# Kernel optimization log

Hardware: AMD Instinct MI355X
Metric: run time of the kernel (lower is better)

Reference implementation:

```python
import jax, jax.numpy as jnp
import numpy as np

T, H, W, B = 9, 128, 128, 8  # size=[9,128,128], 8 samples in batch
N = 4194304


def _avg3(x):
    # AvgPool3d(kernel=(1,3,3), stride=1, pad=(0,1,1), count_include_pad=True)
    s = jax.lax.reduce_window(x, 0.0, jax.lax.add, (1, 1, 1, 3, 3), (1, 1, 1, 1, 1),
                              ((0, 0), (0, 0), (0, 0), (1, 1), (1, 1)))
    return s / 9.0


def _inorm(x, eps=1e-5):
    # InstanceNorm3d(affine=False): normalize over (T,H,W) per sample/channel
    m = x.mean(axis=(2, 3, 4), keepdims=True)
    v = x.var(axis=(2, 3, 4), keepdims=True)
    return (x - m) * jax.lax.rsqrt(v + eps)


def _time_corr(x):
    bx = (x > 0).astype(x.dtype)
    bx = jnp.concatenate([bx, bx[:, :, -1:]], axis=2)  # ReplicationPad3d back in T
    prev = _avg3(bx)
    around = (prev[:, :, :-1] * bx[:, :, 1:] > 4.0 / 9.0).astype(x.dtype)
    return _avg3(around)


def _dyn_conv(x, fc1_w, fc2_w, dyn_w):
    # Dynamic_Conv, kernel (3,1,1): attention over k=4 weight banks, per-sample conv
    a = x.mean(axis=(2, 3, 4))                       # [B,C] global avg pool
    a = jax.nn.relu(a @ fc1_w.T)
    a = jax.nn.softmax(a @ fc2_w.T, axis=1)          # [B,k]
    w = jnp.einsum('bk,koid->boid', a, dyn_w)        # [B,O,I,3]
    xp = jnp.pad(x, ((0, 0), (0, 0), (1, 1), (0, 0), (0, 0)))  # pad T
    t = x.shape[2]
    out = jnp.einsum('boi,bithw->bothw', w[..., 0], xp[:, :, 0:t])
    out = out + jnp.einsum('boi,bithw->bothw', w[..., 1], xp[:, :, 1:1 + t])
    out = out + jnp.einsum('boi,bithw->bothw', w[..., 2], xp[:, :, 2:2 + t])
    return out


def _voxelize(t, x, y, p, b):
    # per-batch normalize t by max, then bilinear-in-time scatter-add over T bins
    tmax = jax.ops.segment_max(t, b, num_segments=B)
    ts = (t / tmax[b]) * T                                         # [N]
    bins = jnp.arange(T, dtype=ts.dtype)
    vals = jnp.maximum(1.0 - jnp.abs(ts[None, :] - bins[:, None]), 0.0)  # [T,N]
    base = x + W * y + W * H * T * p + 2 * W * H * T * b           # [N]
    idx = base[None, :] + W * H * jnp.arange(T, dtype=base.dtype)[:, None]
    vox = jnp.zeros(B * 2 * T * H * W, dtype=ts.dtype).at[idx].add(vals)
    return vox.reshape(B, 2, T, H, W)


def setup_inputs() -> dict:
    key = jax.random.key(0)
    ks = jax.random.split(key, 10)
    t = jax.random.uniform(ks[0], (N,), dtype=jnp.float32)
    x = jax.random.randint(ks[1], (N,), 0, W, dtype=jnp.int32)
    y = jax.random.randint(ks[2], (N,), 0, H, dtype=jnp.int32)
    p = jax.random.randint(ks[3], (N,), 0, 2, dtype=jnp.int32)
    b = jnp.sort(jax.random.randint(ks[4], (N,), 0, B, dtype=jnp.int32))
    conv1_w = jax.random.normal(ks[5], (16, 2), jnp.float32) / np.sqrt(2.0)
    fc1_w = jax.random.normal(ks[6], (8, 16), jnp.float32) / np.sqrt(16.0)
    fc2_w = jax.random.normal(ks[7], (4, 8), jnp.float32) / np.sqrt(8.0)
    dyn_w = jax.random.normal(ks[8], (4, 16, 16, 3), jnp.float32) / np.sqrt(48.0)
    conv3_w = jax.random.normal(ks[9], (2, 16), jnp.float32) / np.sqrt(16.0)
    return {"t": t, "x": x, "y": y, "p": p, "b": b,
            "conv1_w": conv1_w, "fc1_w": fc1_w, "fc2_w": fc2_w,
            "dyn_w": dyn_w, "conv3_w": conv3_w}


def reference(t, x, y, p, b, conv1_w, fc1_w, fc2_w, dyn_w, conv3_w):
    vox = _voxelize(t, x, y, p, b)                     # [B,2,T,H,W]
    mask = _time_corr(vox)
    h = _inorm(vox)
    h = jnp.einsum('oc,bcthw->bothw', conv1_w, h)      # 1x1x1 conv 2->16
    h = _dyn_conv(h, fc1_w, fc2_w, dyn_w)
    h = jnp.einsum('oc,bcthw->bothw', conv3_w, h)      # 1x1x1 conv 16->2
    out = _inorm(jax.nn.sigmoid(h) * mask)
    return out
```

## Files before the change

kernel.cpp:

```cpp
#include <hip/hip_runtime.h>
#include <math.h>

#define TT 9
#define HH 128
#define WW 128
#define BB 8
#define SLICE (HH*WW)
#define CHW (TT*SLICE)
#define BCH (2*CHW)
#define TOT (BB*BCH)
#define INV_M (1.0f/147456.0f)
#define NYG 16
#define NBK (9*NYG)
#define SEGCAP 8192u
#define SSCALE 274877906944.0f
#define INV_SSCALE (1.0/274877906944.0)

__global__ void __launch_bounds__(1024) k_bounds(
        const int* __restrict__ b, int* __restrict__ start, int n,
        const float* __restrict__ conv1_w, const float* __restrict__ dyn_w,
        const float* __restrict__ conv3_w, float* __restrict__ Kc,
        unsigned* __restrict__ tailz, unsigned* __restrict__ cursor, int initCur) {
    if (blockIdx.x == 1) {
        if (threadIdx.x < 72) tailz[threadIdx.x] = 0u;
        if (initCur)
            for (int i = threadIdx.x; i < 8 * NBK; i += 1024)
                cursor[i] = (unsigned)i * SEGCAP;
        return;
    }
    int tid = threadIdx.x;
    if (tid < 9) {
        if (tid == 0) start[0] = 0;
        else if (tid == 8) start[8] = n;
        else {
            int lo = 0, hi = n;
            while (lo < hi) { int mid = (lo + hi) >> 1; if (b[mid] < tid) lo = mid + 1; else hi = mid; }
            start[tid] = lo;
        }
    }
    if (tid >= 32 && tid < 44) {
        int q = tid - 32;
        int d = q % 3, c = (q / 3) & 1, o2 = q / 6;
        float acc = 0.0f;
        for (int o = 0; o < 16; ++o) {
            float c3 = conv3_w[o2 * 16 + o];
            for (int i = 0; i < 16; ++i) {
                float wsum = 0.0f;
                for (int k = 0; k < 4; ++k) wsum += dyn_w[((k * 16 + o) * 16 + i) * 3 + d];
                acc += c3 * (0.25f * wsum) * conv1_w[i * 2 + c];
            }
        }
        Kc[q] = acc;
    }
}

__global__ void __launch_bounds__(1024) k_tmax(
        const float* __restrict__ t, const int* __restrict__ start,
        unsigned* __restrict__ gmax) {
    __shared__ unsigned sm[1024];
    int bi = blockIdx.x & 7, cj = blockIdx.x >> 3, nb = gridDim.x >> 3;
    int s = start[bi], e = start[bi + 1];
    unsigned m = 0u;
    if (e > s) {
        int a = (s + 3) & ~3; if (a > e) a = e;
        int z = e & ~3;       if (z < a) z = a;
        if (cj == 0) {
            int i = s + (int)threadIdx.x;
            if (i < a) { unsigned v = __float_as_uint(t[i]); if (v > m) m = v; }
            i = z + (int)threadIdx.x;
            if (i < e) { unsigned v = __float_as_uint(t[i]); if (v > m) m = v; }
        }
        long nq = (long)(z - a) >> 2;
        long per = (nq + nb - 1) / nb;
        long q0 = (long)cj * per; if (q0 > nq) q0 = nq;
        long q1 = q0 + per;       if (q1 > nq) q1 = nq;
        const float4* tp = (const float4*)(t + a);
        for (long i = q0 + threadIdx.x; i < q1; i += 1024) {
            float4 u = tp[i];
            unsigned c = __float_as_uint(fmaxf(fmaxf(u.x, u.y), fmaxf(u.z, u.w)));
            if (c > m) m = c;
        }
    }
    sm[threadIdx.x] = m;
    __syncthreads();
    for (int ofs = 512; ofs > 0; ofs >>= 1) {
        if (threadIdx.x < ofs && sm[threadIdx.x + ofs] > sm[threadIdx.x])
            sm[threadIdx.x] = sm[threadIdx.x + ofs];
        __syncthreads();
    }
    if (threadIdx.x == 0 && sm[0]) atomicMax(&gmax[bi], sm[0]);
}

__global__ void __launch_bounds__(1024) k_place(
        const float* __restrict__ t, const int* __restrict__ x,
        const int* __restrict__ y, const int* __restrict__ p,
        const unsigned* __restrict__ gmax, const int* __restrict__ start,
        unsigned* __restrict__ cursor, int2* __restrict__ rec) {
    __shared__ unsigned lh[NBK], lc[NBK], cbase[NBK];
    __shared__ unsigned wsum[3];
    __shared__ int2 srec[4096];
    __shared__ unsigned char sbkt[4096];
    int bi = blockIdx.x & 7, cj = blockIdx.x >> 3, nb = gridDim.x >> 3;
    int s = start[bi], e = start[bi + 1];
    if (e <= s) return;
    float tmax = __uint_as_float(gmax[bi]);
    int a = (s + 3) & ~3; if (a > e) a = e;
    int z = e & ~3;       if (z < a) z = a;
    long nq = (long)(z - a) >> 2;
    long per = (nq + nb - 1) / nb;
    long q0 = (long)cj * per; if (q0 > nq) q0 = nq;
    long q1 = q0 + per;       if (q1 > nq) q1 = nq;
    const float4* tp = (const float4*)(t + a);
    const int4*   xp = (const int4*)(x + a);
    const int4*   yp = (const int4*)(y + a);
    const int4*   pp = (const int4*)(p + a);
    for (long base = q0; base < q1; base += 1024) {
        if (threadIdx.x < NBK) lh[threadIdx.x] = 0u;
        __syncthreads();
        long qi = base + threadIdx.x;
        int lb[4]; float tsv[4]; int keyv[4]; unsigned rank[4];
        #pragma unroll
        for (int k = 0; k < 4; ++k) lb[k] = -1;
        if (qi < q1) {
            float4 tv = tp[qi]; int4 xv = xp[qi]; int4 yv = yp[qi]; int4 pv = pp[qi];
            float tq[4] = {tv.x, tv.y, tv.z, tv.w};
            int   xq[4] = {xv.x, xv.y, xv.z, xv.w};
            int   yq[4] = {yv.x, yv.y, yv.z, yv.w};
            int   pq[4] = {pv.x, pv.y, pv.z, pv.w};
            #pragma unroll
            for (int k = 0; k < 4; ++k) {
                float ts = tq[k] / tmax * 9.0f;
                int i0 = (int)floorf(ts);
                if ((unsigned)i0 < 9u) {
                    lb[k] = i0 * NYG + (yq[k] >> 3);
                    tsv[k] = ts;
                    keyv[k] = xq[k] + (yq[k] << 7) + (pq[k] << 14);
                }
            }
        }
        #pragma unroll
        for (int k = 0; k < 4; ++k)
            if (lb[k] >= 0) rank[k] = atomicAdd(&lh[lb[k]], 1u);
        __syncthreads();
        unsigned v = 0, inc = 0;
        if (threadIdx.x < 192) {
            v = (threadIdx.x < NBK) ? lh[threadIdx.x] : 0u;
            inc = v;
            #pragma unroll
            for (int ofs = 1; ofs < 64; ofs <<= 1) {
                unsigned u = __shfl_up(inc, ofs, 64);
                if ((threadIdx.x & 63) >= ofs) inc += u;
            }
            if ((threadIdx.x & 63) == 63) wsum[threadIdx.x >> 6] = inc;
        }
        __syncthreads();
        if (threadIdx.x < NBK) {
            unsigned ex = inc - v;
            int w = threadIdx.x >> 6;
            if (w >= 1) ex += wsum[0];
            if (w >= 2) ex += wsum[1];
            cbase[threadIdx.x] = ex;
            lc[threadIdx.x] = v ? atomicAdd(&cursor[bi * NBK + threadIdx.x], v) : 0u;
        }
        __syncthreads();
        #pragma unroll
        for (int k = 0; k < 4; ++k)
            if (lb[k] >= 0) {
                unsigned sl_ = cbase[lb[k]] + rank[k];
                srec[sl_] = make_int2(__float_as_int(tsv[k]), keyv[k]);
                sbkt[sl_] = (unsigned char)lb[k];
            }
        __syncthreads();
        unsigned tot = cbase[NBK - 1] + lh[NBK - 1];
        #pragma unroll
        for (int h = 0; h < 4; ++h) {
            unsigned slot = threadIdx.x + h * 1024;
            if (slot < tot) {
                int bkt = sbkt[slot];
                unsigned dst = lc[bkt] + (slot - cbase[bkt]);
                if (dst < (unsigned)(bi * NBK + bkt + 1) * SEGCAP)
                    rec[dst] = srec[slot];
            }
        }
        __syncthreads();
    }
    if (cj == 0) {
        int i = -1;
        if ((int)threadIdx.x < a - s) i = s + threadIdx.x;
        else if (threadIdx.x >= 64 && (int)(threadIdx.x - 64) < e - z) i = z + (threadIdx.x - 64);
        if (i >= 0) {
            float ts = t[i] / tmax * 9.0f;
            int i0 = (int)floorf(ts);
            if ((unsigned)i0 < 9u) {
                int lbx = i0 * NYG + (y[i] >> 3);
                unsigned slot = atomicAdd(&cursor[bi * NBK + lbx], 1u);
                if (slot < (unsigned)(bi * NBK + lbx + 1) * SEGCAP)
                    rec[slot] = make_int2(__float_as_int(ts), x[i] + (y[i] << 7) + (p[i] << 14));
            }
        }
    }
}

#define CELL(K) (((K) & 1023) | (((K) >> 4) & 1024))
#define DEP1(TSB, KEY) { float ts_ = __int_as_float(TSB); \
    unsigned long long sq_ = (unsigned long long)(ts_ * SSCALE); \
    atomicAdd(&asl[CELL(KEY)], (1ull << 48) | sq_); }

__global__ void __launch_bounds__(1024) k_accum(
        const int2* __restrict__ rec, const unsigned* __restrict__ cursor,
        unsigned long long* __restrict__ Abuf) {
    __shared__ unsigned long long asl[2048];
    int tg = blockIdx.x, bb = blockIdx.y, yg = blockIdx.z;
    asl[threadIdx.x] = 0ull; asl[1024 + threadIdx.x] = 0ull;
    __syncthreads();
    int lb = bb * NBK + tg * NYG + yg;
    unsigned s = (unsigned)lb * SEGCAP;
    unsigned e = cursor[lb];
    unsigned cap = s + SEGCAP; if (e > cap) e = cap;
    unsigned a = (s + 1) & ~1u, z = e & ~1u; if (z < a) z = a;
    if (threadIdx.x == 0 && s < a && s < e) { int2 r = rec[s]; DEP1(r.x, r.y) }
    if (threadIdx.x == 1 && z < e)          { int2 r = rec[z]; DEP1(r.x, r.y) }
    int n2 = (int)((z - a) >> 1);
    const int4* rp = (const int4*)(rec + a);
    for (int i = threadIdx.x; i < n2; i += 1024) {
        int4 q = rp[i];
        DEP1(q.x, q.y)
        DEP1(q.z, q.w)
    }
    __syncthreads();
    unsigned long long* Ao = Abuf + s;
    Ao[threadIdx.x]        = asl[threadIdx.x];
    Ao[1024 + threadIdx.x] = asl[1024 + threadIdx.x];
}

__global__ void __launch_bounds__(256) k_recon(
        const unsigned long long* __restrict__ Abuf,
        float* __restrict__ vox, float* __restrict__ s1) {
    int idx = blockIdx.x * 256 + threadIdx.x;
    int cell = idx & 2047;
    int yg = (idx >> 11) & 15;
    int bb = idx >> 15;
    unsigned long long Av[9];
    #pragma unroll
    for (int t = 0; t < 9; ++t)
        Av[t] = Abuf[(size_t)(unsigned)(bb * NBK + t * NYG + yg) * SEGCAP + cell];
    int p = cell >> 10, row = (cell >> 7) & 7, xx = cell & 127;
    float* vp = vox + (size_t)bb * BCH + (size_t)p * CHW + (size_t)(((yg << 3) + row) << 7) + xx;
    double Cp = 0.0, Sp = 0.0;
    float ls = 0.f, lq = 0.f;
    #pragma unroll
    for (int t = 0; t < 9; ++t) {
        double C = (double)(unsigned)(Av[t] >> 48);
        double S = (double)(Av[t] & 0xFFFFFFFFFFFFull) * INV_SSCALE;
        float v = (float)(C * (double)(1 + t) - S + (Sp - Cp * (double)(t - 1)));
        vp[t * SLICE] = v;
        ls += v; lq += v * v;
        Cp = C; Sp = S;
    }
    __shared__ float ss[256], sq[256];
    ss[threadIdx.x] = ls; sq[threadIdx.x] = lq;
    __syncthreads();
    for (int ofs = 128; ofs > 0; ofs >>= 1) {
        if (threadIdx.x < ofs) { ss[threadIdx.x] += ss[threadIdx.x + ofs]; sq[threadIdx.x] += sq[threadIdx.x + ofs]; }
        __syncthreads();
    }
    if (threadIdx.x == 0) {
        int bc = bb * 2 + p;
        atomicAdd(&s1[bc], ss[0]); atomicAdd(&s1[16 + bc], sq[0]);
    }
}

__global__ void __launch_bounds__(1024, 4) k_scat(
        const float* __restrict__ t, const int* __restrict__ x,
        const int* __restrict__ y, const int* __restrict__ p,
        const unsigned* __restrict__ gmax, const int* __restrict__ start,
        float* __restrict__ vox) {
    __shared__ float sl[2 * SLICE];
    int tg = blockIdx.x, bb = blockIdx.y;
    int cs = start[bb], ce = start[bb + 1];
    for (int j = threadIdx.x; j < 2 * SLICE; j += 1024) sl[j] = 0.0f;
    __syncthreads();
    float tmax = __uint_as_float(gmax[bb]);
    float ftg = (float)tg;
    for (int i = cs + threadIdx.x; i < ce; i += 1024) {
        float ts = t[i] / tmax * 9.0f;
        float fl = floorf(ts);
        int i0 = (int)fl;
        bool h0 = (i0 == tg), h1 = (i0 + 1 == tg);
        if (h0 | h1) {
            float w = h0 ? (1.0f - (ts - fl)) : (1.0f - (ftg - ts));
            int hw = x[i] + (y[i] << 7) + (p[i] << 14);
            atomicAdd(&sl[hw], w);
        }
    }
    __syncthreads();
    float* dst = vox + (size_t)bb * BCH + (size_t)tg * SLICE;
    for (int j = threadIdx.x; j < SLICE; j += 1024) {
        dst[j]       = sl[j];
        dst[CHW + j] = sl[SLICE + j];
    }
}

__global__ void k_stats1(const float* __restrict__ vox, float* __restrict__ s1) {
    __shared__ float ss[256], sq[256];
    int bc = blockIdx.x >> 5, part = blockIdx.x & 31;
    const float4* vp = (const float4*)(vox + (long)bc * CHW);
    const int per = (CHW / 4) / 32;
    float s = 0.f, q = 0.f;
    for (int j = part * per + threadIdx.x; j < (part + 1) * per; j += 256) {
        float4 v = vp[j];
        s += v.x + v.y + v.z + v.w;
        q += v.x * v.x + v.y * v.y + v.z * v.z + v.w * v.w;
    }
    ss[threadIdx.x] = s; sq[threadIdx.x] = q;
    __syncthreads();
    for (int ofs = 128; ofs > 0; ofs >>= 1) {
        if (threadIdx.x < ofs) { ss[threadIdx.x] += ss[threadIdx.x + ofs]; sq[threadIdx.x] += sq[threadIdx.x + ofs]; }
        __syncthreads();
    }
    if (threadIdx.x == 0) { atomicAdd(&s1[bc], ss[0]); atomicAdd(&s1[16 + bc], sq[0]); }
}

#define STRIP 32
__global__ void k_mask(const float* __restrict__ vox, float* __restrict__ mask) {
    __shared__ unsigned char sbx[36 * 128];
    __shared__ unsigned char sar[34 * 128];
    int bid = blockIdx.x;
    int strip = bid & 3;
    int t = (bid >> 2) % 9;
    int c = (bid / 36) & 1;
    int bb = bid / 72;
    long off = (long)bb * BCH + (long)c * CHW;
    const float* vt = vox + off + (long)t * SLICE;
    int tn = (t + 1 < 9) ? t + 1 : 8;
    const float* vn = vox + off + (long)tn * SLICE;
    int y0 = strip * STRIP;
    for (int j = threadIdx.x; j < 36 * 128; j += 256) {
        int r = j >> 7, xx = j & 127;
        int gy = y0 - 2 + r;
        sbx[j] = ((unsigned)gy < 128u && vt[(gy << 7) + xx] > 0.0f) ? 1 : 0;
    }
    __syncthreads();
    for (int j = threadIdx.x; j < 34 * 128; j += 256) {
        int ra = j >> 7, xx = j & 127;
        int gy = y0 - 1 + ra;
        unsigned char v = 0;
        if ((unsigned)gy < 128u) {
            int s = 0;
            for (int rs = ra; rs <= ra + 2; ++rs)
                for (int dx = -1; dx <= 1; ++dx) {
                    int x2 = xx + dx; if ((unsigned)x2 >= 128u) continue;
                    s += sbx[(rs << 7) + x2];
                }
            v = (vn[(gy << 7) + xx] > 0.0f && s >= 5) ? 1 : 0;
        }
        sar[j] = v;
    }
    __syncthreads();
    float* mt = mask + off + (long)t * SLICE;
    for (int j = threadIdx.x; j < STRIP * 128; j += 256) {
        int q = j >> 7, xx = j & 127;
        int s = 0;
        for (int ra = q; ra <= q + 2; ++ra)
            for (int dx = -1; dx <= 1; ++dx) {
                int x2 = xx + dx; if ((unsigned)x2 >= 128u) continue;
                s += sar[(ra << 7) + x2];
            }
        mt[((y0 + q) << 7) + xx] = (float)s / 9.0f;
    }
}

__global__ void __launch_bounds__(256) k_g(
        const float* __restrict__ vox, float* __restrict__ gm,
        const float* __restrict__ s1, const float* __restrict__ Kc,
        float* __restrict__ s2) {
    __shared__ float snrm[32];
    if (threadIdx.x < 16) {
        float mm = s1[threadIdx.x] * INV_M;
        float var = s1[16 + threadIdx.x] * INV_M - mm * mm;
        float inv = rsqrtf(var + 1e-5f);
        snrm[threadIdx.x] = inv;
        snrm[16 + threadIdx.x] = -mm * inv;
    }
    __syncthreads();
    int idx = blockIdx.x * 256 + threadIdx.x;
    int hw = idx & (SLICE - 1);
    int o2 = (idx >> 14) & 1;
    int bb = idx >> 15;
    const float* v0 = vox + (size_t)bb * BCH + hw;
    const float* v1 = v0 + CHW;
    float* go = gm + (size_t)bb * BCH + (size_t)o2 * CHW + hw;
    float a[9], d[9], m[9];
    #pragma unroll
    for (int tt = 0; tt < 9; ++tt) a[tt] = v0[tt * SLICE];
    #pragma unroll
    for (int tt = 0; tt < 9; ++tt) d[tt] = v1[tt * SLICE];
    #pragma unroll
    for (int tt = 0; tt < 9; ++tt) m[tt] = go[tt * SLICE];
    float sc0 = snrm[bb * 2], sh0 = snrm[16 + bb * 2];
    float sc1 = snrm[bb * 2 + 1], sh1 = snrm[16 + bb * 2 + 1];
    float k00 = Kc[o2 * 6 + 0], k01 = Kc[o2 * 6 + 1], k02 = Kc[o2 * 6 + 2];
    float k10 = Kc[o2 * 6 + 3], k11 = Kc[o2 * 6 + 4], k12 = Kc[o2 * 6 + 5];
    #pragma unroll
    for (int tt = 0; tt < 9; ++tt) { a[tt] = a[tt] * sc0 + sh0; d[tt] = d[tt] * sc1 + sh1; }
    float ls = 0.f, lq = 0.f;
    #pragma unroll
    for (int tt = 0; tt < 9; ++tt) {
        float pre = k01 * a[tt] + k11 * d[tt];
        if (tt > 0) pre += k00 * a[tt - 1] + k10 * d[tt - 1];
        if (tt < 8) pre += k02 * a[tt + 1] + k12 * d[tt + 1];
        float sig = 1.0f / (1.0f + expf(-pre));
        float g = sig * m[tt];
        go[tt * SLICE] = g;
        ls += g; lq += g * g;
    }
    __shared__ float ss[256], sq[256];
    ss[threadIdx.x] = ls; sq[threadIdx.x] = lq;
    __syncthreads();
    for (int ofs = 128; ofs > 0; ofs >>= 1) {
        if (threadIdx.x < ofs) { ss[threadIdx.x] += ss[threadIdx.x + ofs]; sq[threadIdx.x] += sq[threadIdx.x + ofs]; }
        __syncthreads();
    }
    if (threadIdx.x == 0) {
        int bc = bb * 2 + o2;
        atomicAdd(&s2[bc], ss[0]); atomicAdd(&s2[16 + bc], sq[0]);
    }
}

__global__ void k_norm(float* __restrict__ out, const float* __restrict__ s2) {
    int i4 = blockIdx.x * 256 + threadIdx.x;
    int bc = i4 / (CHW / 4);
    float m = s2[bc] * INV_M;
    float var = s2[16 + bc] * INV_M - m * m;
    float inv = rsqrtf(var + 1e-5f);
    float4 v = ((float4*)out)[i4];
    v.x = (v.x - m) * inv; v.y = (v.y - m) * inv;
    v.z = (v.z - m) * inv; v.w = (v.w - m) * inv;
    ((float4*)out)[i4] = v;
}

extern "C" void kernel_launch(void* const* d_in, const int* in_sizes, int n_in,
                              void* d_out, int out_size, void* d_ws, size_t ws_size,
                              hipStream_t stream) {
    const float* t  = (const float*)d_in[0];
    const int*   x  = (const int*)d_in[1];
    const int*   y  = (const int*)d_in[2];
    const int*   p  = (const int*)d_in[3];
    const int*   b  = (const int*)d_in[4];
    const float* conv1_w = (const float*)d_in[5];
    const float* dyn_w   = (const float*)d_in[8];
    const float* conv3_w = (const float*)d_in[9];
    float* out = (float*)d_out;
    int n = in_sizes[0];

    const long RECF = 2L * 8 * NBK * SEGCAP;
    long availF = (long)(ws_size / sizeof(float));
    long need = (long)TOT + RECF + 4096;
    int useBuckets = (availF >= need);

    float* ws   = (float*)d_ws;
    float* vox  = ws;
    int2*  rec  = (int2*)(ws + TOT);
    float* tail = ws + TOT + (useBuckets ? RECF : 0);
    unsigned* gmax    = (unsigned*)tail;
    float*    s1      = tail + 8;
    float*    s2      = tail + 40;
    float*    Kc      = tail + 72;
    int*      start   = (int*)(tail + 84);
    unsigned* cursor  = (unsigned*)(tail + 96);

    k_bounds<<<2, 1024, 0, stream>>>(b, start, n, conv1_w, dyn_w, conv3_w, Kc,
                                     (unsigned*)tail, cursor, useBuckets);
    k_tmax<<<256, 1024, 0, stream>>>(t, start, gmax);
    if (useBuckets) {
        k_place<<<512, 1024, 0, stream>>>(t, x, y, p, gmax, start, cursor, rec);
        k_accum<<<dim3(9, 8, NYG), 1024, 0, stream>>>(rec, cursor,
                                                      (unsigned long long*)rec);
        k_recon<<<1024, 256, 0, stream>>>((const unsigned long long*)rec, vox, s1);
    } else {
        k_scat<<<dim3(9, 8, 1), 1024, 0, stream>>>(t, x, y, p, gmax, start, vox);
        k_stats1<<<512, 256, 0, stream>>>(vox, s1);
    }
    k_mask<<<576, 256, 0, stream>>>(vox, out);
    k_g<<<1024, 256, 0, stream>>>(vox, out, s1, Kc, s2);
    k_norm<<<TOT / 1024, 256, 0, stream>>>(out, s2);
}
```

Measured before the change: 134.8 us.

## Fuse bucket accumulation and voxel reconstruction into one kernel looping over time

Merges k_accum and k_recon into k_accum9. Each block now owns one batch and one 4-row y-group and walks all nine time bins in turn, accumulating into LDS and writing voxel values and partial statistics straight from shared memory. This removes the 64-bit accumulator round trip through global memory and one kernel launch. To fit the LDS tile, bucketing changes to 32 y-groups with half the segment capacity, which means 2-byte bucket ids and a wider prefix scan in k_place. The trade-off is a smaller grid (256 blocks instead of 1152) with serial per-bin loops and extra barriers.

```diff
diff --git a/kernel.cpp b/kernel.cpp
--- a/kernel.cpp
+++ b/kernel.cpp
@@ -10,9 +10,9 @@
 #define BCH (2*CHW)
 #define TOT (BB*BCH)
 #define INV_M (1.0f/147456.0f)
-#define NYG 16
+#define NYG 32
 #define NBK (9*NYG)
-#define SEGCAP 8192u
+#define SEGCAP 4096u
 #define SSCALE 274877906944.0f
 #define INV_SSCALE (1.0/274877906944.0)
 
@@ -97,9 +97,9 @@
         const unsigned* __restrict__ gmax, const int* __restrict__ start,
         unsigned* __restrict__ cursor, int2* __restrict__ rec) {
     __shared__ unsigned lh[NBK], lc[NBK], cbase[NBK];
-    __shared__ unsigned wsum[3];
+    __shared__ unsigned wsum[5];
     __shared__ int2 srec[4096];
-    __shared__ unsigned char sbkt[4096];
+    __shared__ unsigned short sbkt[4096];
     int bi = blockIdx.x & 7, cj = blockIdx.x >> 3, nb = gridDim.x >> 3;
     int s = start[bi], e = start[bi + 1];
     if (e <= s) return;
@@ -132,7 +132,7 @@
                 float ts = tq[k] / tmax * 9.0f;
                 int i0 = (int)floorf(ts);
                 if ((unsigned)i0 < 9u) {
-                    lb[k] = i0 * NYG + (yq[k] >> 3);
+                    lb[k] = i0 * NYG + (yq[k] >> 2);
                     tsv[k] = ts;
                     keyv[k] = xq[k] + (yq[k] << 7) + (pq[k] << 14);
                 }
@@ -143,7 +143,7 @@
             if (lb[k] >= 0) rank[k] = atomicAdd(&lh[lb[k]], 1u);
         __syncthreads();
         unsigned v = 0, inc = 0;
-        if (threadIdx.x < 192) {
+        if (threadIdx.x < 320) {
             v = (threadIdx.x < NBK) ? lh[threadIdx.x] : 0u;
             inc = v;
             #pragma unroll
@@ -157,8 +157,7 @@
         if (threadIdx.x < NBK) {
             unsigned ex = inc - v;
             int w = threadIdx.x >> 6;
-            if (w >= 1) ex += wsum[0];
-            if (w >= 2) ex += wsum[1];
+            for (int j = 0; j < w; ++j) ex += wsum[j];
             cbase[threadIdx.x] = ex;
             lc[threadIdx.x] = v ? atomicAdd(&cursor[bi * NBK + threadIdx.x], v) : 0u;
         }
@@ -168,7 +167,7 @@
             if (lb[k] >= 0) {
                 unsigned sl_ = cbase[lb[k]] + rank[k];
                 srec[sl_] = make_int2(__float_as_int(tsv[k]), keyv[k]);
-                sbkt[sl_] = (unsigned char)lb[k];
+                sbkt[sl_] = (unsigned short)lb[k];
             }
         __syncthreads();
         unsigned tot = cbase[NBK - 1] + lh[NBK - 1];
@@ -192,7 +191,7 @@
             float ts = t[i] / tmax * 9.0f;
             int i0 = (int)floorf(ts);
             if ((unsigned)i0 < 9u) {
-                int lbx = i0 * NYG + (y[i] >> 3);
+                int lbx = i0 * NYG + (y[i] >> 2);
                 unsigned slot = atomicAdd(&cursor[bi * NBK + lbx], 1u);
                 if (slot < (unsigned)(bi * NBK + lbx + 1) * SEGCAP)
                     rec[slot] = make_int2(__float_as_int(ts), x[i] + (y[i] << 7) + (p[i] << 14));
@@ -201,73 +200,61 @@
     }
 }
 
-#define CELL(K) (((K) & 1023) | (((K) >> 4) & 1024))
+#define CELL(K) (((K) & 511) | (((K) >> 5) & 512))
 #define DEP1(TSB, KEY) { float ts_ = __int_as_float(TSB); \
     unsigned long long sq_ = (unsigned long long)(ts_ * SSCALE); \
     atomicAdd(&asl[CELL(KEY)], (1ull << 48) | sq_); }
 
-__global__ void __launch_bounds__(1024) k_accum(
+__global__ void __launch_bounds__(1024) k_accum9(
         const int2* __restrict__ rec, const unsigned* __restrict__ cursor,
-        unsigned long long* __restrict__ Abuf) {
-    __shared__ unsigned long long asl[2048];
-    int tg = blockIdx.x, bb = blockIdx.y, yg = blockIdx.z;
-    asl[threadIdx.x] = 0ull; asl[1024 + threadIdx.x] = 0ull;
-    __syncthreads();
-    int lb = bb * NBK + tg * NYG + yg;
-    unsigned s = (unsigned)lb * SEGCAP;
-    unsigned e = cursor[lb];
-    unsigned cap = s + SEGCAP; if (e > cap) e = cap;
-    unsigned a = (s + 1) & ~1u, z = e & ~1u; if (z < a) z = a;
-    if (threadIdx.x == 0 && s < a && s < e) { int2 r = rec[s]; DEP1(r.x, r.y) }
-    if (threadIdx.x == 1 && z < e)          { int2 r = rec[z]; DEP1(r.x, r.y) }
-    int n2 = (int)((z - a) >> 1);
-    const int4* rp = (const int4*)(rec + a);
-    for (int i = threadIdx.x; i < n2; i += 1024) {
-        int4 q = rp[i];
-        DEP1(q.x, q.y)
-        DEP1(q.z, q.w)
-    }
-    __syncthreads();
-    unsigned long long* Ao = Abuf + s;
-    Ao[threadIdx.x]        = asl[threadIdx.x];
-    Ao[1024 + threadIdx.x] = asl[1024 + threadIdx.x];
-}
-
-__global__ void __launch_bounds__(256) k_recon(
-        const unsigned long long* __restrict__ Abuf,
         float* __restrict__ vox, float* __restrict__ s1) {
-    int idx = blockIdx.x * 256 + threadIdx.x;
-    int cell = idx & 2047;
-    int yg = (idx >> 11) & 15;
-    int bb = idx >> 15;
-    unsigned long long Av[9];
-    #pragma unroll
-    for (int t = 0; t < 9; ++t)
-        Av[t] = Abuf[(size_t)(unsigned)(bb * NBK + t * NYG + yg) * SEGCAP + cell];
-    int p = cell >> 10, row = (cell >> 7) & 7, xx = cell & 127;
-    float* vp = vox + (size_t)bb * BCH + (size_t)p * CHW + (size_t)(((yg << 3) + row) << 7) + xx;
+    __shared__ unsigned long long asl[1024];
+    __shared__ float rs[1024], rq[1024];
+    int bb = blockIdx.x, yg = blockIdx.y;
+    int cell = threadIdx.x;
+    int pch = cell >> 9, row = (cell >> 7) & 3, xx = cell & 127;
+    float* vp = vox + (size_t)bb * BCH + (size_t)pch * CHW
+              + (size_t)(((yg << 2) + row) << 7) + xx;
     double Cp = 0.0, Sp = 0.0;
     float ls = 0.f, lq = 0.f;
-    #pragma unroll
     for (int t = 0; t < 9; ++t) {
-        double C = (double)(unsigned)(Av[t] >> 48);
-        double S = (double)(Av[t] & 0xFFFFFFFFFFFFull) * INV_SSCALE;
+        asl[cell] = 0ull;
+        __syncthreads();
+        int lb = bb * NBK + t * NYG + yg;
+        unsigned s = (unsigned)lb * SEGCAP;
+        unsigned e = cursor[lb];
+        unsigned cap = s + SEGCAP; if (e > cap) e = cap;
+        unsigned a = (s + 1) & ~1u, z = e & ~1u; if (z < a) z = a;
+        if (threadIdx.x == 0 && s < a && s < e) { int2 r = rec[s]; DEP1(r.x, r.y) }
+        if (threadIdx.x == 1 && z < e)          { int2 r = rec[z]; DEP1(r.x, r.y) }
+        int n2 = (int)((z - a) >> 1);
+        const int4* rp = (const int4*)(rec + a);
+        for (int i = threadIdx.x; i < n2; i += 1024) {
+            int4 q = rp[i];
+            DEP1(q.x, q.y)
+            DEP1(q.z, q.w)
+        }
+        __syncthreads();
+        unsigned long long Av = asl[cell];
+        double C = (double)(unsigned)(Av >> 48);
+        double S = (double)(Av & 0xFFFFFFFFFFFFull) * INV_SSCALE;
         float v = (float)(C * (double)(1 + t) - S + (Sp - Cp * (double)(t - 1)));
         vp[t * SLICE] = v;
         ls += v; lq += v * v;
         Cp = C; Sp = S;
-    }
-    __shared__ float ss[256], sq[256];
-    ss[threadIdx.x] = ls; sq[threadIdx.x] = lq;
-    __syncthreads();
-    for (int ofs = 128; ofs > 0; ofs >>= 1) {
-        if (threadIdx.x < ofs) { ss[threadIdx.x] += ss[threadIdx.x + ofs]; sq[threadIdx.x] += sq[threadIdx.x + ofs]; }
-        __syncthreads();
-    }
-    if (threadIdx.x == 0) {
-        int bc = bb * 2 + p;
-        atomicAdd(&s1[bc], ss[0]); atomicAdd(&s1[16 + bc], sq[0]);
-    }
+        __syncthreads();
+    }
+    rs[threadIdx.x] = ls; rq[threadIdx.x] = lq;
+    __syncthreads();
+    for (int ofs = 256; ofs > 0; ofs >>= 1) {
+        if ((threadIdx.x & 511) < ofs) {
+            rs[threadIdx.x] += rs[threadIdx.x + ofs];
+            rq[threadIdx.x] += rq[threadIdx.x + ofs];
+        }
+        __syncthreads();
+    }
+    if (threadIdx.x == 0)   { atomicAdd(&s1[bb * 2],     rs[0]);   atomicAdd(&s1[16 + bb * 2],     rq[0]); }
+    if (threadIdx.x == 512) { atomicAdd(&s1[bb * 2 + 1], rs[512]); atomicAdd(&s1[16 + bb * 2 + 1], rq[512]); }
 }
 
 __global__ void __launch_bounds__(1024, 4) k_scat(
@@ -455,7 +442,7 @@
 
     const long RECF = 2L * 8 * NBK * SEGCAP;
     long availF = (long)(ws_size / sizeof(float));
-    long need = (long)TOT + RECF + 4096;
+    long need = (long)TOT + RECF + 8192;
     int useBuckets = (availF >= need);
 
     float* ws   = (float*)d_ws;
@@ -474,9 +461,7 @@
     k_tmax<<<256, 1024, 0, stream>>>(t, start, gmax);
     if (useBuckets) {
         k_place<<<512, 1024, 0, stream>>>(t, x, y, p, gmax, start, cursor, rec);
-        k_accum<<<dim3(9, 8, NYG), 1024, 0, stream>>>(rec, cursor,
-                                                      (unsigned long long*)rec);
-        k_recon<<<1024, 256, 0, stream>>>((const unsigned long long*)rec, vox, s1);
+        k_accum9<<<dim3(8, NYG), 1024, 0, stream>>>(rec, cursor, vox, s1);
     } else {
         k_scat<<<dim3(9, 8, 1), 1024, 0, stream>>>(t, x, y, p, gmax, start, vox);
         k_stats1<<<512, 256, 0, stream>>>(vox, s1);
```

Result: faster. 125.9 us (median of 2 runs) (-6.6%).
